# Optimization experiments

Measured on AMD Instinct MI355X. Metric: run time of the kernel, lower is better.

The kernel has to match this reference:

```python
import jax, jax.numpy as jnp
import numpy as np

BETA = 1e-8
ALPHA = 0.5
CHOOSE_K = 128
MEMORY_SIZE = 65536
KEY_DIM = 256
BATCH = 1024


def _l2norm(x, axis=-1, eps=1e-12):
    return x / jnp.sqrt(jnp.sum(x * x, axis=axis, keepdims=True) + eps)


def setup_inputs() -> dict:
    key = jax.random.key(0)
    k1, k2, k3 = jax.random.split(key, 3)
    q = _l2norm(jax.random.normal(k1, (BATCH, KEY_DIM), dtype=jnp.float32))
    memory_key = _l2norm(jax.random.normal(k2, (MEMORY_SIZE, KEY_DIM), dtype=jnp.float32))
    # module init: hist[:] = 1e-5; add small random variation so topk is non-degenerate
    memory_hist = 1e-5 + 1e-3 * jax.random.uniform(k3, (MEMORY_SIZE,), dtype=jnp.float32)
    # module init: values = ones, second half zeroed
    memory_values = jnp.concatenate([
        jnp.ones((MEMORY_SIZE // 2,), dtype=jnp.float32),
        jnp.zeros((MEMORY_SIZE - MEMORY_SIZE // 2,), dtype=jnp.float32),
    ])
    return {"q": q, "memory_key": memory_key,
            "memory_hist": memory_hist, "memory_values": memory_values}


def reference(q, memory_key, memory_hist, memory_values):
    # obtain_topk over FULL memory: dense similarity [B, M]
    sims = jnp.matmul(q, memory_key.T)                      # [B, M]
    scores = jnp.exp(sims - 1.0) * (memory_hist + BETA)[None, :]
    _, k_idxs = jax.lax.top_k(scores, CHOOSE_K)             # [B, K]

    # gather reduced memory at topk indices
    red_keys = memory_key[k_idxs]                           # [B, K, D]
    red_hist = memory_hist[k_idxs] * ALPHA                  # [B, K]
    red_vals = memory_values[k_idxs]                        # [B, K]

    # posterior over the K gathered slots
    sim_k = jnp.einsum('bd,bkd->bk', q, red_keys)           # [B, K]
    joint = jnp.exp(sim_k - 1.0) * (red_hist + BETA)        # [B, K]
    posterior = joint / jnp.sum(joint, axis=1, keepdims=True)
    result = jnp.sum(posterior * red_vals, axis=1)          # [B]
    return result
```

## Files before the change

### kernel.cpp

```cpp
#include <hip/hip_runtime.h>

#define BATCH   1024
#define MSIZE   65536
#define KDIM    256
#define CHOOSEK 128
#define SELK    160
#define BETA    1e-8f
#define ALPHA   0.5f
#define KSC  425.0f
#define KOFF 7.2f

typedef short bf16x8 __attribute__((ext_vector_type(8)));
typedef float f32x4  __attribute__((ext_vector_type(4)));

__device__ inline unsigned int pack2bf(float a, float b) {
    unsigned int ua = __float_as_uint(a);
    unsigned int ub = __float_as_uint(b);
    ua += 0x7fffu + ((ua >> 16) & 1u);
    ub += 0x7fffu + ((ub >> 16) & 1u);
    return (ua >> 16) | (ub & 0xffff0000u);
}

#define GLD16(g, l) __builtin_amdgcn_global_load_lds( \
    (const __attribute__((address_space(1))) unsigned int*)(g), \
    (__attribute__((address_space(3))) unsigned int*)(l), 16, 0, 0)

__global__ __launch_bounds__(256)
void convert_kernel(const float* __restrict__ q, const float* __restrict__ key,
                    const float* __restrict__ hist,
                    unsigned short* __restrict__ qs, unsigned short* __restrict__ kb,
                    float* __restrict__ Ltab)
{
    const int bid = blockIdx.x, tid = threadIdx.x;
    if (bid < 8192) {
        const int off = bid * 256 + tid;
        const float4* s4 = (const float4*)key;
        float4 a = s4[off * 2], b = s4[off * 2 + 1];
        ((uint4*)kb)[off] = make_uint4(pack2bf(a.x, a.y), pack2bf(a.z, a.w),
                                       pack2bf(b.x, b.y), pack2bf(b.z, b.w));
    } else if (bid < 8320) {
        const int f = (bid - 8192) * 256 + tid;
        const int l = f & 63, j = (f >> 6) & 3, ks = (f >> 8) & 7;
        const int wmg = (f >> 11) & 1, bt = f >> 12;
        const int r = bt * 128 + wmg * 64 + j * 16 + (l & 15);
        const int c = ks * 32 + (l >> 4) * 8;
        const float* src = q + (size_t)r * KDIM + c;
        float4 a = *(const float4*)src, b = *(const float4*)(src + 4);
        ((uint4*)qs)[f] = make_uint4(pack2bf(a.x, a.y), pack2bf(a.z, a.w),
                                     pack2bf(b.x, b.y), pack2bf(b.z, b.w));
    } else {
        const int n = (bid - 8320) * 256 + tid;
        Ltab[n] = (logf(hist[n] + BETA) + KOFF) * KSC;
    }
}

__global__ __launch_bounds__(256, 3)
void score_kernel(const unsigned short* __restrict__ qs,
                  const unsigned short* __restrict__ kb,
                  const float* __restrict__ Ltab,
                  unsigned char* __restrict__ s8)
{
    __shared__ __align__(16) unsigned short Bs[3][128 * 32];
    const int tid = threadIdx.x;
    const int bid = blockIdx.x;
    const int b0 = ((bid >> 3) & 7) * 128;
    const int n0 = ((bid & 7) + ((bid >> 6) << 3)) * 128;
    const int lane = tid & 63, wave = tid >> 6;
    const int wm = (wave >> 1) * 64, wn = (wave & 1) * 64;
    const int l15 = lane & 15, l4 = lane >> 4;
    const int bt = (bid >> 3) & 7, wmg = wave >> 1;

    f32x4 acc[4][4] = {};

    const int srow = tid >> 2;
    const int seg  = (tid & 3) * 8;
    const unsigned short* gB = kb + (size_t)(n0 + srow) * KDIM + seg;
    const int lofs = srow * 32 + seg;

    const bf16x8* qw = (const bf16x8*)qs + ((bt * 2 + wmg) * 8) * 4 * 64 + lane;

#define STAGE_B(st) do {                                             \
    const int _ko = (st) * 32;                                       \
    GLD16(gB + _ko,             &Bs[(st) % 3][lofs]);                \
    GLD16(gB + _ko + 64 * KDIM, &Bs[(st) % 3][lofs + 64 * 32]);     \
} while (0)

#define STEP(s, WN) do {                                                     \
    asm volatile("s_waitcnt vmcnt(" #WN ")" ::: "memory");                   \
    __builtin_amdgcn_s_barrier();                                            \
    asm volatile("" ::: "memory");                                           \
    bf16x8 qf[4];                                                            \
    _Pragma("unroll")                                                        \
    for (int j = 0; j < 4; ++j) qf[j] = qw[(((s) * 4 + j) * 64)];            \
    if ((s) + 2 < 8) STAGE_B((s) + 2);                                       \
    bf16x8 kf[4];                                                            \
    _Pragma("unroll")                                                        \
    for (int i = 0; i < 4; ++i)                                              \
        kf[i] = *(const bf16x8*)(&Bs[(s) % 3][(wn + i * 16 + l15) * 32 + l4 * 8]); \
    _Pragma("unroll")                                                        \
    for (int i = 0; i < 4; ++i)                                              \
        _Pragma("unroll")                                                    \
        for (int j = 0; j < 4; ++j)                                          \
            acc[i][j] = __builtin_amdgcn_mfma_f32_16x16x32_bf16(kf[i], qf[j], acc[i][j], 0, 0, 0); \
} while (0)

    STAGE_B(0); STAGE_B(1);

    STEP(0, 2); STEP(1, 2); STEP(2, 2); STEP(3, 2);
    STEP(4, 2); STEP(5, 2); STEP(6, 2); STEP(7, 0);

#undef STEP
#undef STAGE_B

    float4 Lv[4];
#pragma unroll
    for (int i = 0; i < 4; ++i)
        Lv[i] = *(const float4*)&Ltab[n0 + wn + i * 16 + l4 * 4];
#pragma unroll
    for (int j = 0; j < 4; ++j) {
        const size_t row = (size_t)(b0 + wm + j * 16 + l15) * MSIZE;
#pragma unroll
        for (int i = 0; i < 4; ++i) {
            const float* lv = (const float*)&Lv[i];
            unsigned int pk = 0;
#pragma unroll
            for (int reg = 0; reg < 4; ++reg) {
                float x = fmaf(acc[i][j][reg], KSC, lv[reg]);
                x = fminf(fmaxf(x, 0.0f), 255.0f);
                pk |= (unsigned int)(int)x << (8 * reg);
            }
            *(unsigned int*)(s8 + row + (n0 + wn + i * 16 + l4 * 4)) = pk;
        }
    }
}

__global__ __launch_bounds__(256, 4)
void select_kernel(const float* __restrict__ q,
                   const float* __restrict__ key,
                   const float* __restrict__ hist,
                   const float* __restrict__ vals,
                   const unsigned char* __restrict__ s8,
                   float* __restrict__ out)
{
    const int b   = blockIdx.x;
    const int tid = threadIdx.x;

    __shared__ __align__(16) float qs[KDIM];
    __shared__ unsigned int hcnt[16 * 257];
    __shared__ int   stot[256];
    __shared__ int   scal[2];
    __shared__ int   cidx[1024];
    __shared__ float csc[1024], cjj[1024], cjv[1024];
    __shared__ float wred[8];

    qs[tid] = q[(size_t)b * KDIM + tid];
    const uint4* rowp = reinterpret_cast<const uint4*>(s8 + (size_t)b * MSIZE);
    const int rep = (tid & 15) * 257;

    int H = -1;
    int minb = 128;
    for (;;) {
        for (int i = tid; i < 16 * 257; i += 256) hcnt[i] = 0u;
        if (tid == 0) { scal[0] = -1; scal[1] = 0; }
        __syncthreads();

        for (int i = 0; i < 16; ++i) {
            uint4 v = rowp[i * 256 + tid];
            unsigned int w[4] = {v.x, v.y, v.z, v.w};
#pragma unroll
            for (int k = 0; k < 4; ++k) {
                if (minb == 0 || (w[k] & 0x80808080u)) {
#pragma unroll
                    for (int jj = 0; jj < 4; ++jj) {
                        int bb = (int)((w[k] >> (8 * jj)) & 0xffu);
                        if (bb >= minb) atomicAdd(&hcnt[rep + bb], 1u);
                    }
                }
            }
        }
        __syncthreads();
        { unsigned int t = 0;
#pragma unroll
          for (int k = 0; k < 16; ++k) t += hcnt[k * 257 + tid];
          stot[tid] = (int)t; }
        __syncthreads();

        if (tid < 64) {
            const int l = tid;
            int t0 = stot[l * 4], t1 = stot[l * 4 + 1], t2 = stot[l * 4 + 2], t3 = stot[l * 4 + 3];
            int lsum = t0 + t1 + t2 + t3;
            int s = lsum;
#pragma unroll
            for (int off = 1; off < 64; off <<= 1) {
                int u = __shfl_down(s, off, 64);
                if (l + off < 64) s += u;
            }
            int A  = s - lsum;
            int S3 = A + t3;
            int S2 = S3 + t2;
            int S1 = S2 + t1;
            int S0 = S1 + t0;
            if (S0 >= SELK && S1 < SELK) scal[0] = l * 4 + 0;
            if (S1 >= SELK && S2 < SELK) scal[0] = l * 4 + 1;
            if (S2 >= SELK && S3 < SELK) scal[0] = l * 4 + 2;
            if (S3 >= SELK && A  < SELK) scal[0] = l * 4 + 3;
        }
        __syncthreads();
        H = scal[0];
        __syncthreads();
        if (H >= 0) break;
        minb = 0;
    }

    const unsigned int uH = (unsigned int)H;
    const bool pre = (H >= 128);
    for (int i = 0; i < 16; ++i) {
        uint4 v = rowp[i * 256 + tid];
        const int base = (i * 256 + tid) * 16;
        unsigned int w[4] = {v.x, v.y, v.z, v.w};
#pragma unroll
        for (int k = 0; k < 4; ++k) {
            if (!pre || (w[k] & 0x80808080u)) {
#pragma unroll
                for (int jj = 0; jj < 4; ++jj) {
                    unsigned int bb = (w[k] >> (8 * jj)) & 0xffu;
                    if (bb >= uH) {
                        int p = atomicAdd(&scal[1], 1);
                        if (p < 1024) cidx[p] = base + 4 * k + jj;
                    }
                }
            }
        }
    }
    __syncthreads();
    const int ncand = min(scal[1], 1024);

    const int gid = tid >> 4, gl = tid & 15;
    const float4* q4 = (const float4*)qs;
    for (int i = gid; i < ncand; i += 16) {
        const int idx = cidx[i];
        const float4* kp = (const float4*)(key + (size_t)idx * KDIM);
        float p = 0.f;
#pragma unroll
        for (int u = 0; u < 4; ++u) {
            float4 kk = kp[gl * 4 + u];
            float4 qq = q4[gl * 4 + u];
            p += kk.x * qq.x + kk.y * qq.y + kk.z * qq.z + kk.w * qq.w;
        }
#pragma unroll
        for (int off = 1; off < 16; off <<= 1) p += __shfl_xor(p, off, 64);
        if (gl == 0) {
            float e = expf(p - 1.0f);
            float h = hist[idx];
            csc[i] = e * (h + BETA);
            float j = e * (ALPHA * h + BETA);
            cjj[i] = j;
            cjv[i] = j * vals[idx];
        }
    }
    __syncthreads();

    const int wave = tid >> 6, lane = tid & 63;
    float pn = 0.f, pd = 0.f;
    for (int i = tid; i < ncand; i += 256) {
        float si = csc[i]; int ii = cidx[i]; int rank = 0;
        for (int t = 0; t < ncand; ++t) {
            float st = csc[t];
            rank += (st > si || (st == si && cidx[t] < ii)) ? 1 : 0;
        }
        if (rank < CHOOSEK) { pn += cjv[i]; pd += cjj[i]; }
    }
#pragma unroll
    for (int off = 32; off > 0; off >>= 1) {
        pn += __shfl_xor(pn, off, 64);
        pd += __shfl_xor(pd, off, 64);
    }
    if (lane == 0) { wred[wave] = pn; wred[4 + wave] = pd; }
    __syncthreads();
    if (tid == 0) {
        float n = wred[0] + wred[1] + wred[2] + wred[3];
        float d = wred[4] + wred[5] + wred[6] + wred[7];
        out[b] = n / d;
    }
}

extern "C" void kernel_launch(void* const* d_in, const int* in_sizes, int n_in,
                              void* d_out, int out_size, void* d_ws, size_t ws_size,
                              hipStream_t stream)
{
    (void)in_sizes; (void)n_in; (void)out_size; (void)ws_size;
    const float* q    = (const float*)d_in[0];
    const float* key  = (const float*)d_in[1];
    const float* hist = (const float*)d_in[2];
    const float* vals = (const float*)d_in[3];
    float* out = (float*)d_out;

    unsigned char*  s8 = (unsigned char*)d_ws;
    unsigned short* kb = (unsigned short*)((char*)d_ws + ((size_t)64 << 20));
    unsigned short* qsw= (unsigned short*)((char*)d_ws + ((size_t)96 << 20));
    float*          Lt = (float*)((char*)d_ws + ((size_t)96 << 20) + (512 << 10));

    convert_kernel<<<8576, 256, 0, stream>>>(q, key, hist, qsw, kb, Lt);
    score_kernel<<<4096, 256, 0, stream>>>(qsw, kb, Lt, s8);
    select_kernel<<<BATCH, 256, 0, stream>>>(q, key, hist, vals, s8, out);
}
```

Measured before the change: 212.8 us.

## Enlarge score tile to 256 batch rows and cache candidate word list in select

The score kernel now runs 512-thread blocks covering 256 batch rows per 128-key tile, so each staged key tile in LDS is shared by eight waves instead of four, halving key-tile traffic. Q fragments are double-buffered in registers, with raised wave priority around the MFMA block, and the Q swizzle layout in the convert kernel is updated to match. The select kernel records which 32-bit words contained high-byte scores during the histogram pass, then rescans only those words to collect candidates instead of reading the whole row again. This trades more registers per thread and a 4KB LDS list (with a full-scan fallback on overflow) for less global and LDS traffic.

Result: no change. 210.9 us (-0.9%).

```diff
diff --git a/kernel.cpp b/kernel.cpp
--- a/kernel.cpp
+++ b/kernel.cpp
@@ -41,8 +41,8 @@
     } else if (bid < 8320) {
         const int f = (bid - 8192) * 256 + tid;
         const int l = f & 63, j = (f >> 6) & 3, ks = (f >> 8) & 7;
-        const int wmg = (f >> 11) & 1, bt = f >> 12;
-        const int r = bt * 128 + wmg * 64 + j * 16 + (l & 15);
+        const int wmg = (f >> 11) & 3, bt = (f >> 13) & 3;
+        const int r = bt * 256 + wmg * 64 + j * 16 + (l & 15);
         const int c = ks * 32 + (l >> 4) * 8;
         const float* src = q + (size_t)r * KDIM + c;
         float4 a = *(const float4*)src, b = *(const float4*)(src + 4);
@@ -54,7 +54,7 @@
     }
 }
 
-__global__ __launch_bounds__(256, 3)
+__global__ __launch_bounds__(512, 4)
 void score_kernel(const unsigned short* __restrict__ qs,
                   const unsigned short* __restrict__ kb,
                   const float* __restrict__ Ltab,
@@ -63,12 +63,13 @@
     __shared__ __align__(16) unsigned short Bs[3][128 * 32];
     const int tid = threadIdx.x;
     const int bid = blockIdx.x;
-    const int b0 = ((bid >> 3) & 7) * 128;
-    const int n0 = ((bid & 7) + ((bid >> 6) << 3)) * 128;
+    const int bt = (bid >> 3) & 3;
+    const int b0 = bt * 256;
+    const int n0 = ((bid & 7) + ((bid >> 5) << 3)) * 128;
     const int lane = tid & 63, wave = tid >> 6;
     const int wm = (wave >> 1) * 64, wn = (wave & 1) * 64;
     const int l15 = lane & 15, l4 = lane >> 4;
-    const int bt = (bid >> 3) & 7, wmg = wave >> 1;
+    const int wmg = wave >> 1;
 
     f32x4 acc[4][4] = {};
 
@@ -77,37 +78,41 @@
     const unsigned short* gB = kb + (size_t)(n0 + srow) * KDIM + seg;
     const int lofs = srow * 32 + seg;
 
-    const bf16x8* qw = (const bf16x8*)qs + ((bt * 2 + wmg) * 8) * 4 * 64 + lane;
-
-#define STAGE_B(st) do {                                             \
-    const int _ko = (st) * 32;                                       \
-    GLD16(gB + _ko,             &Bs[(st) % 3][lofs]);                \
-    GLD16(gB + _ko + 64 * KDIM, &Bs[(st) % 3][lofs + 64 * 32]);     \
+    const bf16x8* qw = (const bf16x8*)qs + (size_t)((bt * 4 + wmg) * 32) * 64 + lane;
+
+    bf16x8 qf[2][4];
+
+#define STAGE_B(st) GLD16(gB + (st) * 32, &Bs[(st) % 3][lofs])
+
+#define STEP(s, WN) do {                                                          \
+    asm volatile("s_waitcnt vmcnt(" #WN ")" ::: "memory");                        \
+    __builtin_amdgcn_s_barrier();                                                 \
+    asm volatile("" ::: "memory");                                                \
+    if ((s) < 7) {                                                                \
+        _Pragma("unroll")                                                         \
+        for (int j = 0; j < 4; ++j)                                               \
+            qf[((s) + 1) & 1][j] = qw[(((s) + 1) * 4 + j) * 64];                  \
+    }                                                                             \
+    if ((s) + 2 < 8) STAGE_B((s) + 2);                                            \
+    bf16x8 kf[4];                                                                 \
+    _Pragma("unroll")                                                             \
+    for (int i = 0; i < 4; ++i)                                                   \
+        kf[i] = *(const bf16x8*)(&Bs[(s) % 3][(wn + i * 16 + l15) * 32 + l4 * 8]);\
+    __builtin_amdgcn_s_setprio(1);                                                \
+    _Pragma("unroll")                                                             \
+    for (int i = 0; i < 4; ++i)                                                   \
+        _Pragma("unroll")                                                         \
+        for (int j = 0; j < 4; ++j)                                               \
+            acc[i][j] = __builtin_amdgcn_mfma_f32_16x16x32_bf16(kf[i], qf[(s) & 1][j], acc[i][j], 0, 0, 0); \
+    __builtin_amdgcn_s_setprio(0);                                                \
 } while (0)
 
-#define STEP(s, WN) do {                                                     \
-    asm volatile("s_waitcnt vmcnt(" #WN ")" ::: "memory");                   \
-    __builtin_amdgcn_s_barrier();                                            \
-    asm volatile("" ::: "memory");                                           \
-    bf16x8 qf[4];                                                            \
-    _Pragma("unroll")                                                        \
-    for (int j = 0; j < 4; ++j) qf[j] = qw[(((s) * 4 + j) * 64)];            \
-    if ((s) + 2 < 8) STAGE_B((s) + 2);                                       \
-    bf16x8 kf[4];                                                            \
-    _Pragma("unroll")                                                        \
-    for (int i = 0; i < 4; ++i)                                              \
-        kf[i] = *(const bf16x8*)(&Bs[(s) % 3][(wn + i * 16 + l15) * 32 + l4 * 8]); \
-    _Pragma("unroll")                                                        \
-    for (int i = 0; i < 4; ++i)                                              \
-        _Pragma("unroll")                                                    \
-        for (int j = 0; j < 4; ++j)                                          \
-            acc[i][j] = __builtin_amdgcn_mfma_f32_16x16x32_bf16(kf[i], qf[j], acc[i][j], 0, 0, 0); \
-} while (0)
-
+#pragma unroll
+    for (int j = 0; j < 4; ++j) qf[0][j] = qw[j * 64];
     STAGE_B(0); STAGE_B(1);
 
-    STEP(0, 2); STEP(1, 2); STEP(2, 2); STEP(3, 2);
-    STEP(4, 2); STEP(5, 2); STEP(6, 2); STEP(7, 0);
+    STEP(0, 1); STEP(1, 1); STEP(2, 1); STEP(3, 1);
+    STEP(4, 1); STEP(5, 1); STEP(6, 1); STEP(7, 0);
 
 #undef STEP
 #undef STAGE_B
@@ -148,20 +153,22 @@
     __shared__ __align__(16) float qs[KDIM];
     __shared__ unsigned int hcnt[16 * 257];
     __shared__ int   stot[256];
-    __shared__ int   scal[2];
+    __shared__ int   scal[3];
+    __shared__ unsigned short wlist[2048];
     __shared__ int   cidx[1024];
     __shared__ float csc[1024], cjj[1024], cjv[1024];
     __shared__ float wred[8];
 
     qs[tid] = q[(size_t)b * KDIM + tid];
     const uint4* rowp = reinterpret_cast<const uint4*>(s8 + (size_t)b * MSIZE);
+    const unsigned int* roww = reinterpret_cast<const unsigned int*>(rowp);
     const int rep = (tid & 15) * 257;
 
-    int H = -1;
+    int H = -1, nw = 0;
     int minb = 128;
     for (;;) {
         for (int i = tid; i < 16 * 257; i += 256) hcnt[i] = 0u;
-        if (tid == 0) { scal[0] = -1; scal[1] = 0; }
+        if (tid == 0) { scal[0] = -1; scal[1] = 0; scal[2] = 0; }
         __syncthreads();
 
         for (int i = 0; i < 16; ++i) {
@@ -170,6 +177,10 @@
 #pragma unroll
             for (int k = 0; k < 4; ++k) {
                 if (minb == 0 || (w[k] & 0x80808080u)) {
+                    if (minb) {
+                        int p = atomicAdd(&scal[2], 1);
+                        if (p < 2048) wlist[p] = (unsigned short)((i * 256 + tid) * 4 + k);
+                    }
 #pragma unroll
                     for (int jj = 0; jj < 4; ++jj) {
                         int bb = (int)((w[k] >> (8 * jj)) & 0xffu);
@@ -206,27 +217,42 @@
             if (S3 >= SELK && A  < SELK) scal[0] = l * 4 + 3;
         }
         __syncthreads();
-        H = scal[0];
+        H = scal[0]; nw = scal[2];
         __syncthreads();
         if (H >= 0) break;
         minb = 0;
     }
 
     const unsigned int uH = (unsigned int)H;
-    const bool pre = (H >= 128);
-    for (int i = 0; i < 16; ++i) {
-        uint4 v = rowp[i * 256 + tid];
-        const int base = (i * 256 + tid) * 16;
-        unsigned int w[4] = {v.x, v.y, v.z, v.w};
-#pragma unroll
-        for (int k = 0; k < 4; ++k) {
-            if (!pre || (w[k] & 0x80808080u)) {
-#pragma unroll
-                for (int jj = 0; jj < 4; ++jj) {
-                    unsigned int bb = (w[k] >> (8 * jj)) & 0xffu;
-                    if (bb >= uH) {
-                        int p = atomicAdd(&scal[1], 1);
-                        if (p < 1024) cidx[p] = base + 4 * k + jj;
+    if (minb != 0 && nw <= 2048) {
+        for (int i = tid; i < nw; i += 256) {
+            const int wi = (int)wlist[i];
+            unsigned int w = roww[wi];
+#pragma unroll
+            for (int jj = 0; jj < 4; ++jj) {
+                unsigned int bb = (w >> (8 * jj)) & 0xffu;
+                if (bb >= uH) {
+                    int p = atomicAdd(&scal[1], 1);
+                    if (p < 1024) cidx[p] = wi * 4 + jj;
+                }
+            }
+        }
+    } else {
+        const bool pre = (H >= 128);
+        for (int i = 0; i < 16; ++i) {
+            uint4 v = rowp[i * 256 + tid];
+            const int base = (i * 256 + tid) * 16;
+            unsigned int w[4] = {v.x, v.y, v.z, v.w};
+#pragma unroll
+            for (int k = 0; k < 4; ++k) {
+                if (!pre || (w[k] & 0x80808080u)) {
+#pragma unroll
+                    for (int jj = 0; jj < 4; ++jj) {
+                        unsigned int bb = (w[k] >> (8 * jj)) & 0xffu;
+                        if (bb >= uH) {
+                            int p = atomicAdd(&scal[1], 1);
+                            if (p < 1024) cidx[p] = base + 4 * k + jj;
+                        }
                     }
                 }
             }
@@ -301,6 +327,6 @@
     float*          Lt = (float*)((char*)d_ws + ((size_t)96 << 20) + (512 << 10));
 
     convert_kernel<<<8576, 256, 0, stream>>>(q, key, hist, qsw, kb, Lt);
-    score_kernel<<<4096, 256, 0, stream>>>(qsw, kb, Lt, s8);
+    score_kernel<<<2048, 512, 0, stream>>>(qsw, kb, Lt, s8);
     select_kernel<<<BATCH, 256, 0, stream>>>(q, key, hist, vals, s8, out);
 }
```
